# Kernel optimization log

Hardware: AMD Instinct MI355X
Metric: run time of the kernel (lower is better)

## Reference

```python
import jax, jax.numpy as jnp
import numpy as np

B, N, M, F_DIM, H, D = 4, 2048, 2048, 512, 8, 64  # M == num_time
MID = H * D
EPS = 1e-5


def _layernorm(x, w, b):
    mu = jnp.mean(x, axis=-1, keepdims=True)
    var = jnp.var(x, axis=-1, keepdims=True)
    return (x - mu) * jax.lax.rsqrt(var + EPS) * w + b


def setup_inputs() -> dict:
    key = jax.random.key(0)
    ks = jax.random.split(key, 12)
    s = 0.02
    return {
        "x": jax.random.normal(ks[0], (B, N, F_DIM), jnp.float32),
        "context": jax.random.normal(ks[1], (B, M, F_DIM), jnp.float32),
        "pos_emb": jax.random.normal(ks[2], (M, F_DIM), jnp.float32) * s,  # nn.Embedding(num_time, features)
        "ln_w": jnp.ones((F_DIM,), jnp.float32),
        "ln_b": jnp.zeros((F_DIM,), jnp.float32),
        "lnc_w": jnp.ones((F_DIM,), jnp.float32),
        "lnc_b": jnp.zeros((F_DIM,), jnp.float32),
        "Wq": jax.random.normal(ks[3], (F_DIM, MID), jnp.float32) * s,
        "Wk": jax.random.normal(ks[4], (F_DIM, MID), jnp.float32) * s,
        "Wv": jax.random.normal(ks[5], (F_DIM, MID), jnp.float32) * s,
        "Wout": jax.random.normal(ks[6], (MID, F_DIM), jnp.float32) * s,
        "bout": jnp.zeros((F_DIM,), jnp.float32),
    }


def reference(x, context, pos_emb, ln_w, ln_b, lnc_w, lnc_b, Wq, Wk, Wv, Wout, bout):
    scale = D ** (-0.5)
    keys = jnp.broadcast_to(pos_emb[None], (x.shape[0], M, F_DIM))  # [B, T, F]
    xn = _layernorm(x, ln_w, ln_b)
    kn = _layernorm(keys, ln_w, ln_b)          # same norm as x (self.norm)
    cn = _layernorm(context, lnc_w, lnc_b)
    q = (xn @ Wq).reshape(x.shape[0], N, H, D).transpose(0, 2, 1, 3)  # b h n d
    k = (kn @ Wk).reshape(x.shape[0], M, H, D).transpose(0, 2, 1, 3)  # b h m d
    v = (cn @ Wv).reshape(x.shape[0], M, H, D).transpose(0, 2, 1, 3)  # b h m d
    sim = jnp.einsum('bhnd,bhmd->bhnm', q, k) * scale
    attn = jax.nn.softmax(sim, axis=-1)
    out = jnp.einsum('bhnm,bhmd->bhnd', attn, v)
    out = out.transpose(0, 2, 1, 3).reshape(x.shape[0], N, MID)  # b n (h d)
    return out @ Wout + bout
```

## Files before the change

kernel.cpp:

```cpp
#include <hip/hip_runtime.h>
#include <stdint.h>

#define B_ 4
#define N_ 2048
#define M_ 2048
#define F_ 512
#define H_ 8
#define D_ 64

typedef __bf16 bf16x8 __attribute__((ext_vector_type(8)));
typedef float f32x4 __attribute__((ext_vector_type(4)));
typedef float f32x16 __attribute__((ext_vector_type(16)));

typedef const __attribute__((address_space(1))) uint32_t* gas_ptr;
typedef __attribute__((address_space(3))) uint32_t* las_ptr;

__device__ inline ushort f32_bf16(float f) {
    union { float f; uint32_t u; } v; v.f = f;
    uint32_t r = v.u + 0x7FFFu + ((v.u >> 16) & 1u);
    return (ushort)(r >> 16);
}

__global__ __launch_bounds__(128) void ln_kernel(
    const float* __restrict__ x, const float* __restrict__ ctx, const float* __restrict__ pos,
    const float* __restrict__ lnw, const float* __restrict__ lnb,
    const float* __restrict__ lncw, const float* __restrict__ lncb,
    ushort* __restrict__ xn, ushort* __restrict__ kn, ushort* __restrict__ cn)
{
    int r = blockIdx.x;
    const float* src; ushort* dst; const float* w; const float* bp;
    if (r < B_ * N_) {
        src = x + (size_t)r * F_; dst = xn + (size_t)r * F_; w = lnw; bp = lnb;
    } else if (r < B_ * N_ + M_) {
        int rr = r - B_ * N_;
        src = pos + (size_t)rr * F_; dst = kn + (size_t)rr * F_; w = lnw; bp = lnb;
    } else {
        int rr = r - (B_ * N_ + M_);
        src = ctx + (size_t)rr * F_; dst = cn + (size_t)rr * F_; w = lncw; bp = lncb;
    }
    int tid = threadIdx.x;
    int wave = tid >> 6, lane = tid & 63;
    float4 v = reinterpret_cast<const float4*>(src)[tid];
    float s = v.x + v.y + v.z + v.w;
    float sq = v.x * v.x + v.y * v.y + v.z * v.z + v.w * v.w;
    #pragma unroll
    for (int mask = 1; mask < 64; mask <<= 1) {
        s += __shfl_xor(s, mask, 64);
        sq += __shfl_xor(sq, mask, 64);
    }
    __shared__ float red[4];
    if (lane == 0) { red[wave * 2] = s; red[wave * 2 + 1] = sq; }
    __syncthreads();
    float S = red[0] + red[2], SQ = red[1] + red[3];
    float mean = S * (1.0f / F_);
    float var = SQ * (1.0f / F_) - mean * mean;
    float rstd = rsqrtf(var + 1e-5f);
    float4 wv = reinterpret_cast<const float4*>(w)[tid];
    float4 bv = reinterpret_cast<const float4*>(bp)[tid];
    ushort4 o;
    o.x = f32_bf16((v.x - mean) * rstd * wv.x + bv.x);
    o.y = f32_bf16((v.y - mean) * rstd * wv.y + bv.y);
    o.z = f32_bf16((v.z - mean) * rstd * wv.z + bv.z);
    o.w = f32_bf16((v.w - mean) * rstd * wv.w + bv.w);
    reinterpret_cast<ushort4*>(dst)[tid] = o;
}

__global__ __launch_bounds__(256) void wtrans_kernel(
    const float* __restrict__ Wq, const float* __restrict__ Wk,
    const float* __restrict__ Wv, const float* __restrict__ Wo,
    ushort* __restrict__ WqT, ushort* __restrict__ WkT,
    ushort* __restrict__ WvT, ushort* __restrict__ WoT)
{
    const float* W; ushort* WT;
    switch (blockIdx.z) {
        case 0: W = Wq; WT = WqT; break;
        case 1: W = Wk; WT = WkT; break;
        case 2: W = Wv; WT = WvT; break;
        default: W = Wo; WT = WoT; break;
    }
    __shared__ float tile[32][33];
    int tx = threadIdx.x, ty = threadIdx.y;
    int n0 = blockIdx.x * 32, k0 = blockIdx.y * 32;
    #pragma unroll
    for (int j = 0; j < 4; ++j)
        tile[ty + j * 8][tx] = W[(size_t)(k0 + ty + j * 8) * F_ + n0 + tx];
    __syncthreads();
    #pragma unroll
    for (int j = 0; j < 4; ++j)
        WT[(size_t)(n0 + ty + j * 8) * F_ + k0 + tx] = f32_bf16(tile[tx][ty + j * 8]);
}

__device__ __forceinline__ void gemm_body(
    const ushort* __restrict__ A, const ushort* __restrict__ BT,
    const float* __restrict__ bias, void* __restrict__ Cout,
    int mode, int bx, int by)
{
    __shared__ ushort As[128][64];
    __shared__ ushort Bs[128][64];
    int tid = threadIdx.x;
    int row0 = by * 128, col0 = bx * 128;
    int wv = tid >> 6, lane = tid & 63;
    int wm = wv >> 1, wn = wv & 1;
    f32x4 acc[4][4] = {};

    const int lrow8 = lane >> 3;
    const int chs = ((lane & 7) ^ (lrow8 & 7)) * 8;
    const ushort* agp = A + (size_t)(row0 + wv * 32 + lrow8) * F_ + chs;
    const ushort* bgp = BT + (size_t)(col0 + wv * 32 + lrow8) * F_ + chs;

    for (int k0 = 0; k0 < F_; k0 += 64) {
        #pragma unroll
        for (int j = 0; j < 4; ++j) {
            __builtin_amdgcn_global_load_lds(
                (gas_ptr)(const void*)(agp + k0 + j * 8 * F_),
                (las_ptr)(void*)&As[wv * 32 + j * 8][0], 16, 0, 0);
            __builtin_amdgcn_global_load_lds(
                (gas_ptr)(const void*)(bgp + k0 + j * 8 * F_),
                (las_ptr)(void*)&Bs[wv * 32 + j * 8][0], 16, 0, 0);
        }
        __syncthreads();
        #pragma unroll
        for (int kt = 0; kt < 2; ++kt) {
            int lrow = lane & 15;
            int ch = ((kt * 4 + (lane >> 4)) ^ (lane & 7)) * 8;
            bf16x8 af[4], bfr[4];
            #pragma unroll
            for (int mt = 0; mt < 4; ++mt)
                af[mt] = *reinterpret_cast<const bf16x8*>(&As[wm * 64 + mt * 16 + lrow][ch]);
            #pragma unroll
            for (int nt = 0; nt < 4; ++nt)
                bfr[nt] = *reinterpret_cast<const bf16x8*>(&Bs[wn * 64 + nt * 16 + lrow][ch]);
            #pragma unroll
            for (int mt = 0; mt < 4; ++mt)
                #pragma unroll
                for (int nt = 0; nt < 4; ++nt)
                    acc[mt][nt] = __builtin_amdgcn_mfma_f32_16x16x32_bf16(
                        af[mt], bfr[nt], acc[mt][nt], 0, 0, 0);
        }
        __syncthreads();
    }

    int lr4 = (lane >> 4) * 4, lc = lane & 15;
    #pragma unroll
    for (int mt = 0; mt < 4; ++mt) {
        #pragma unroll
        for (int nt = 0; nt < 4; ++nt) {
            int ccol = col0 + wn * 64 + nt * 16 + lc;
            float bv = (mode == 1) ? bias[ccol] : 0.0f;
            #pragma unroll
            for (int j = 0; j < 4; ++j) {
                int crow = row0 + wm * 64 + mt * 16 + lr4 + j;
                float val = acc[mt][nt][j] + bv;
                if (mode == 1) {
                    reinterpret_cast<float*>(Cout)[(size_t)crow * F_ + ccol] = val;
                } else if (mode == 0) {
                    reinterpret_cast<ushort*>(Cout)[(size_t)crow * F_ + ccol] = f32_bf16(val);
                } else if (mode == 2) {
                    int h = ccol >> 6, t = crow >> 7, s = (crow >> 6) & 1;
                    int ab = (crow >> 5) & 1, l31 = crow & 31;
                    int ds = (ccol >> 4) & 3, g2 = (ccol >> 3) & 1, e = ccol & 7;
                    size_t addr = (((size_t)(h * 16 + t) * 16 + s * 8 + ds * 2 + ab) * 64
                                   + g2 * 32 + l31) * 8 + e;
                    reinterpret_cast<ushort*>(Cout)[addr] = f32_bf16(val);
                } else {
                    int b2 = crow >> 11, m = crow & 2047;
                    int h = ccol >> 6, d = ccol & 63;
                    int bh = b2 * 8 + h, hh = d >> 5, l31 = d & 31;
                    int t = m >> 7, s = (m >> 6) & 1, s_ = (m >> 4) & 3;
                    int g2 = (m >> 3) & 1, i = m & 7;
                    size_t addr = (((size_t)(bh * 16 + t) * 16 + hh * 8 + s * 4 + s_) * 64
                                   + g2 * 32 + l31) * 8 + i;
                    reinterpret_cast<ushort*>(Cout)[addr] = f32_bf16(val);
                }
            }
        }
    }
}

__global__ __launch_bounds__(256) void qkv_gemm_kernel(
    const ushort* __restrict__ xn, const ushort* __restrict__ kn,
    const ushort* __restrict__ cn,
    const ushort* __restrict__ WqT, const ushort* __restrict__ WkT,
    const ushort* __restrict__ WvT,
    ushort* __restrict__ qb, ushort* __restrict__ kF, ushort* __restrict__ vF)
{
    int bid = blockIdx.x;
    if (bid < 256) {
        gemm_body(xn, WqT, nullptr, (void*)qb, 0, bid & 3, bid >> 2);
    } else if (bid < 320) {
        int t = bid - 256;
        gemm_body(kn, WkT, nullptr, (void*)kF, 2, t & 3, t >> 2);
    } else {
        int t = bid - 320;
        gemm_body(cn, WvT, nullptr, (void*)vF, 3, t & 3, t >> 2);
    }
}

__global__ __launch_bounds__(256) void out_gemm_kernel(
    const ushort* __restrict__ A, const ushort* __restrict__ WoT,
    const float* __restrict__ bias, float* __restrict__ out)
{
    gemm_body(A, WoT, bias, (void*)out, 1, blockIdx.x & 3, blockIdx.x >> 2);
}

#define MAKE_PA(dst, p, ss) do {                                               \
    uint32_t w0_, w1_, w2_, w3_;                                               \
    asm("v_cvt_pk_bf16_f32 %0, %1, %2" : "=v"(w0_) : "v"(p[8*(ss)+0]), "v"(p[8*(ss)+1])); \
    asm("v_cvt_pk_bf16_f32 %0, %1, %2" : "=v"(w1_) : "v"(p[8*(ss)+2]), "v"(p[8*(ss)+3])); \
    asm("v_cvt_pk_bf16_f32 %0, %1, %2" : "=v"(w2_) : "v"(p[8*(ss)+4]), "v"(p[8*(ss)+5])); \
    asm("v_cvt_pk_bf16_f32 %0, %1, %2" : "=v"(w3_) : "v"(p[8*(ss)+6]), "v"(p[8*(ss)+7])); \
    asm("v_permlane32_swap_b32 %0, %1" : "+v"(w0_), "+v"(w2_));                \
    asm("v_permlane32_swap_b32 %0, %1" : "+v"(w1_), "+v"(w3_));                \
    union { uint32_t w[4]; bf16x8 v; } u_;                                     \
    u_.w[0] = w0_; u_.w[1] = w1_; u_.w[2] = w2_; u_.w[3] = w3_;                \
    dst = u_.v;                                                                \
} while (0)

#define KLOAD(DST, u) do {                                                     \
    const ushort* _p = kfb_ + (size_t)(u) * 4096 + lane * 8;                   \
    _Pragma("unroll")                                                          \
    for (int f_ = 0; f_ < 8; ++f_)                                             \
        DST[f_] = *reinterpret_cast<const bf16x8*>(_p + f_ * 512);             \
} while (0)

#define VLOAD(DST, u) do {                                                     \
    const ushort* _p = vfb_ + (size_t)((u) >> 1) * 8192 +                      \
                       ((u) & 1) * 4 * 512 + lane * 8;                         \
    _Pragma("unroll")                                                          \
    for (int hh_ = 0; hh_ < 2; ++hh_)                                          \
        _Pragma("unroll")                                                      \
        for (int s2_ = 0; s2_ < 4; ++s2_)                                      \
            DST[hh_ * 4 + s2_] = *reinterpret_cast<const bf16x8*>(             \
                _p + (hh_ * 8 + s2_) * 512);                                   \
} while (0)

#define COMPUTE(KR, VR) do {                                                   \
    f32x16 sA, sB;                                                             \
    _Pragma("unroll")                                                          \
    for (int j = 0; j < 16; ++j) { sA[j] = 0.0f; sB[j] = 0.0f; }               \
    __builtin_amdgcn_s_setprio(1);                                             \
    _Pragma("unroll")                                                          \
    for (int ds_ = 0; ds_ < 4; ++ds_) {                                        \
        sA = __builtin_amdgcn_mfma_f32_32x32x16_bf16(KR[ds_ * 2], qf[ds_], sA, 0, 0, 0); \
        sB = __builtin_amdgcn_mfma_f32_32x32x16_bf16(KR[ds_ * 2 + 1], qf[ds_], sB, 0, 0, 0); \
    }                                                                          \
    __builtin_amdgcn_s_setprio(0);                                             \
    float p0f[16], p1f[16];                                                    \
    _Pragma("unroll")                                                          \
    for (int j = 0; j < 16; ++j)                                               \
        p0f[j] = __builtin_amdgcn_exp2f(sA[j] * c1);                           \
    _Pragma("unroll")                                                          \
    for (int j = 0; j < 16; ++j)                                               \
        p1f[j] = __builtin_amdgcn_exp2f(sB[j] * c1);                           \
    float r0 = 0.0f, r1 = 0.0f, r2 = 0.0f, r3 = 0.0f;                          \
    _Pragma("unroll")                                                          \
    for (int j = 0; j < 16; j += 4) {                                          \
        r0 += p0f[j];     r1 += p0f[j + 1];                                    \
        r2 += p0f[j + 2]; r3 += p0f[j + 3];                                    \
    }                                                                          \
    _Pragma("unroll")                                                          \
    for (int j = 0; j < 16; j += 4) {                                          \
        r0 += p1f[j];     r1 += p1f[j + 1];                                    \
        r2 += p1f[j + 2]; r3 += p1f[j + 3];                                    \
    }                                                                          \
    l_run += (r0 + r1) + (r2 + r3);                                            \
    bf16x8 pa[4];                                                               \
    MAKE_PA(pa[0], p0f, 0);                                                    \
    MAKE_PA(pa[1], p0f, 1);                                                    \
    MAKE_PA(pa[2], p1f, 0);                                                    \
    MAKE_PA(pa[3], p1f, 1);                                                    \
    __builtin_amdgcn_s_setprio(1);                                             \
    _Pragma("unroll")                                                          \
    for (int hh = 0; hh < 2; ++hh)                                             \
        _Pragma("unroll")                                                      \
        for (int s_ = 0; s_ < 4; ++s_)                                         \
            oacc[hh] = __builtin_amdgcn_mfma_f32_32x32x16_bf16(                \
                pa[s_], VR[hh * 4 + s_], oacc[hh], 0, 0, 0);                   \
    __builtin_amdgcn_s_setprio(0);                                             \
} while (0)

__global__ __launch_bounds__(512, 2) void attn_kernel(
    const ushort* __restrict__ q,
    const ushort* __restrict__ kF,
    const ushort* __restrict__ vF,
    ushort* __restrict__ o)
{
    const int wave = threadIdx.x >> 6, lane = threadIdx.x & 63;
    const int l31 = lane & 31, g = lane >> 5;
    const int qsub = wave & 1, quarter = wave >> 1;
    const int bh = blockIdx.y, b = bh >> 3, h = bh & 7;
    const int q0 = blockIdx.x * 64 + qsub * 32;

    __shared__ float ols[2][2][32][64];
    __shared__ float lls[2][2][64];

    bf16x8 qf[4];
    const ushort* qrow = q + (size_t)(b * N_ + q0 + l31) * F_ + h * 64 + g * 8;
    #pragma unroll
    for (int ds = 0; ds < 4; ++ds)
        qf[ds] = *reinterpret_cast<const bf16x8*>(qrow + ds * 16);

    float l_run = 0.0f;
    f32x16 oacc[2];
    #pragma unroll
    for (int hh = 0; hh < 2; ++hh)
        #pragma unroll
        for (int j = 0; j < 16; ++j) oacc[hh][j] = 0.0f;

    const ushort* kfb_ = kF + (size_t)h * 16 * 16 * 512;
    const ushort* vfb_ = vF + (size_t)bh * 16 * 16 * 512;
    const float c1 = 0.18033688f;

    bf16x8 kR[8], vR[8];
    const int ubase = quarter * 8;

    #pragma unroll 1
    for (int uu = 0; uu < 8; ++uu) {
        int u = ubase + uu;
        KLOAD(kR, u);
        VLOAD(vR, u);
        COMPUTE(kR, vR);
    }

    float lfull = l_run + __shfl_xor(l_run, 32, 64);

    if (quarter & 1) {
        int slot = quarter >> 1;
        #pragma unroll
        for (int hh = 0; hh < 2; ++hh)
            #pragma unroll
            for (int j = 0; j < 16; ++j)
                ols[qsub][slot][hh * 16 + j][lane] = oacc[hh][j];
        lls[qsub][slot][lane] = lfull;
    }
    __syncthreads();
    if (!(quarter & 1)) {
        int slot = quarter >> 1;
        #pragma unroll
        for (int hh = 0; hh < 2; ++hh)
            #pragma unroll
            for (int j = 0; j < 16; ++j)
                oacc[hh][j] += ols[qsub][slot][hh * 16 + j][lane];
        lfull += lls[qsub][slot][lane];
    }
    __syncthreads();
    if (quarter == 2) {
        #pragma unroll
        for (int hh = 0; hh < 2; ++hh)
            #pragma unroll
            for (int j = 0; j < 16; ++j)
                ols[qsub][0][hh * 16 + j][lane] = oacc[hh][j];
        lls[qsub][0][lane] = lfull;
    }
    __syncthreads();
    if (quarter == 0) {
        #pragma unroll
        for (int hh = 0; hh < 2; ++hh)
            #pragma unroll
            for (int j = 0; j < 16; ++j)
                oacc[hh][j] += ols[qsub][0][hh * 16 + j][lane];
        lfull += lls[qsub][0][lane];
        float linv = 1.0f / lfull;
        float rli[16];
        #pragma unroll
        for (int j = 0; j < 16; ++j)
            rli[j] = __shfl(linv, 8 * (j >> 2) + 4 * g + (j & 3), 64);
        #pragma unroll
        for (int hh = 0; hh < 2; ++hh)
            #pragma unroll
            for (int j = 0; j < 16; ++j) {
                int qr = (j & 3) + 8 * (j >> 2) + 4 * g;
                o[(size_t)(b * N_ + q0 + qr) * F_ + h * 64 + hh * 32 + l31] =
                    f32_bf16(oacc[hh][j] * rli[j]);
            }
    }
}

extern "C" void kernel_launch(void* const* d_in, const int* in_sizes, int n_in,
                              void* d_out, int out_size, void* d_ws, size_t ws_size,
                              hipStream_t stream) {
    const float* x    = (const float*)d_in[0];
    const float* ctx  = (const float*)d_in[1];
    const float* pos  = (const float*)d_in[2];
    const float* lnw  = (const float*)d_in[3];
    const float* lnb  = (const float*)d_in[4];
    const float* lncw = (const float*)d_in[5];
    const float* lncb = (const float*)d_in[6];
    const float* Wq   = (const float*)d_in[7];
    const float* Wk   = (const float*)d_in[8];
    const float* Wv   = (const float*)d_in[9];
    const float* Wo   = (const float*)d_in[10];
    const float* bout = (const float*)d_in[11];
    float* out = (float*)d_out;

    char* ws = (char*)d_ws;
    ushort* xn  = (ushort*)(ws + 0);
    ushort* cn  = (ushort*)(ws + 8388608);
    ushort* kn  = (ushort*)(ws + 16777216);
    ushort* WqT = (ushort*)(ws + 18874368);
    ushort* WkT = (ushort*)(ws + 19398656);
    ushort* WvT = (ushort*)(ws + 19922944);
    ushort* WoT = (ushort*)(ws + 20447232);
    ushort* qb  = (ushort*)(ws + 20971520);
    ushort* kFb = (ushort*)(ws + 29360128);
    ushort* vFb = (ushort*)(ws + 39845888);
    ushort* ao  = (ushort*)(ws + 48234496);

    hipLaunchKernelGGL(ln_kernel, dim3(B_ * N_ + M_ + B_ * M_), dim3(128), 0, stream,
                       x, ctx, pos, lnw, lnb, lncw, lncb, xn, kn, cn);
    hipLaunchKernelGGL(wtrans_kernel, dim3(16, 16, 4), dim3(32, 8), 0, stream,
                       Wq, Wk, Wv, Wo, WqT, WkT, WvT, WoT);
    hipLaunchKernelGGL(qkv_gemm_kernel, dim3(576), dim3(256), 0, stream,
                       xn, kn, cn, WqT, WkT, WvT, qb, kFb, vFb);
    hipLaunchKernelGGL(attn_kernel, dim3(32, 32), dim3(512), 0, stream,
                       qb, kFb, vFb, ao);
    hipLaunchKernelGGL(out_gemm_kernel, dim3(256), dim3(256), 0, stream,
                       ao, WoT, bout, out);
}
```

Baseline: 108.7 us.

## Process two 32-row query tiles per wave to reuse K/V fragments

Each wave now holds two 32-row query fragments and runs the QK/PV compute for both on every K/V fragment it loads. This halves K/V global loads per query row. Waves split the key range into two halves instead of four, and the cross-wave reduction drops from three barrier stages to one. Each block now covers 256 queries, so the grid shrinks from 32x32 to 8x32 blocks. The price is higher register pressure (two accumulators, the launch_bounds occupancy hint removed) and fewer blocks, which may cut occupancy and load balance across CUs.

Result: faster. 104.0 us (-4.3%).

```diff
diff --git a/kernel.cpp b/kernel.cpp
--- a/kernel.cpp
+++ b/kernel.cpp
@@ -234,15 +234,15 @@
                 _p + (hh_ * 8 + s2_) * 512);                                   \
 } while (0)
 
-#define COMPUTE(KR, VR) do {                                                   \
+#define COMPUTE_ONE(QF, OACC, LR) do {                                         \
     f32x16 sA, sB;                                                             \
     _Pragma("unroll")                                                          \
     for (int j = 0; j < 16; ++j) { sA[j] = 0.0f; sB[j] = 0.0f; }               \
     __builtin_amdgcn_s_setprio(1);                                             \
     _Pragma("unroll")                                                          \
     for (int ds_ = 0; ds_ < 4; ++ds_) {                                        \
-        sA = __builtin_amdgcn_mfma_f32_32x32x16_bf16(KR[ds_ * 2], qf[ds_], sA, 0, 0, 0); \
-        sB = __builtin_amdgcn_mfma_f32_32x32x16_bf16(KR[ds_ * 2 + 1], qf[ds_], sB, 0, 0, 0); \
+        sA = __builtin_amdgcn_mfma_f32_32x32x16_bf16(kR[ds_ * 2], QF[ds_], sA, 0, 0, 0); \
+        sB = __builtin_amdgcn_mfma_f32_32x32x16_bf16(kR[ds_ * 2 + 1], QF[ds_], sB, 0, 0, 0); \
     }                                                                          \
     __builtin_amdgcn_s_setprio(0);                                             \
     float p0f[16], p1f[16];                                                    \
@@ -263,8 +263,8 @@
         r0 += p1f[j];     r1 += p1f[j + 1];                                    \
         r2 += p1f[j + 2]; r3 += p1f[j + 3];                                    \
     }                                                                          \
-    l_run += (r0 + r1) + (r2 + r3);                                            \
-    bf16x8 pa[4];                                                               \
+    LR += (r0 + r1) + (r2 + r3);                                               \
+    bf16x8 pa[4];                                                              \
     MAKE_PA(pa[0], p0f, 0);                                                    \
     MAKE_PA(pa[1], p0f, 1);                                                    \
     MAKE_PA(pa[2], p1f, 0);                                                    \
@@ -274,12 +274,12 @@
     for (int hh = 0; hh < 2; ++hh)                                             \
         _Pragma("unroll")                                                      \
         for (int s_ = 0; s_ < 4; ++s_)                                         \
-            oacc[hh] = __builtin_amdgcn_mfma_f32_32x32x16_bf16(                \
-                pa[s_], VR[hh * 4 + s_], oacc[hh], 0, 0, 0);                   \
+            OACC[hh] = __builtin_amdgcn_mfma_f32_32x32x16_bf16(                \
+                pa[s_], vR[hh * 4 + s_], OACC[hh], 0, 0, 0);                   \
     __builtin_amdgcn_s_setprio(0);                                             \
 } while (0)
 
-__global__ __launch_bounds__(512, 2) void attn_kernel(
+__global__ __launch_bounds__(512) void attn_kernel(
     const ushort* __restrict__ q,
     const ushort* __restrict__ kF,
     const ushort* __restrict__ vF,
@@ -287,91 +287,87 @@
 {
     const int wave = threadIdx.x >> 6, lane = threadIdx.x & 63;
     const int l31 = lane & 31, g = lane >> 5;
-    const int qsub = wave & 1, quarter = wave >> 1;
+    const int qpair = wave & 3, half = wave >> 2;
     const int bh = blockIdx.y, b = bh >> 3, h = bh & 7;
-    const int q0 = blockIdx.x * 64 + qsub * 32;
-
-    __shared__ float ols[2][2][32][64];
-    __shared__ float lls[2][2][64];
-
-    bf16x8 qf[4];
-    const ushort* qrow = q + (size_t)(b * N_ + q0 + l31) * F_ + h * 64 + g * 8;
-    #pragma unroll
-    for (int ds = 0; ds < 4; ++ds)
-        qf[ds] = *reinterpret_cast<const bf16x8*>(qrow + ds * 16);
-
-    float l_run = 0.0f;
-    f32x16 oacc[2];
+    const int q0 = blockIdx.x * 256 + qpair * 64;
+
+    __shared__ float ols[4][64][64];
+    __shared__ float lls[4][2][64];
+
+    bf16x8 qfA[4], qfB[4];
+    const ushort* qrowA = q + (size_t)(b * N_ + q0 + l31) * F_ + h * 64 + g * 8;
+    const ushort* qrowB = qrowA + 32 * F_;
+    #pragma unroll
+    for (int ds = 0; ds < 4; ++ds) {
+        qfA[ds] = *reinterpret_cast<const bf16x8*>(qrowA + ds * 16);
+        qfB[ds] = *reinterpret_cast<const bf16x8*>(qrowB + ds * 16);
+    }
+
+    float l0 = 0.0f, l1 = 0.0f;
+    f32x16 oaccA[2], oaccB[2];
     #pragma unroll
     for (int hh = 0; hh < 2; ++hh)
         #pragma unroll
-        for (int j = 0; j < 16; ++j) oacc[hh][j] = 0.0f;
+        for (int j = 0; j < 16; ++j) { oaccA[hh][j] = 0.0f; oaccB[hh][j] = 0.0f; }
 
     const ushort* kfb_ = kF + (size_t)h * 16 * 16 * 512;
     const ushort* vfb_ = vF + (size_t)bh * 16 * 16 * 512;
     const float c1 = 0.18033688f;
 
     bf16x8 kR[8], vR[8];
-    const int ubase = quarter * 8;
+    const int ubase = half * 16;
 
     #pragma unroll 1
-    for (int uu = 0; uu < 8; ++uu) {
+    for (int uu = 0; uu < 16; ++uu) {
         int u = ubase + uu;
         KLOAD(kR, u);
         VLOAD(vR, u);
-        COMPUTE(kR, vR);
-    }
-
-    float lfull = l_run + __shfl_xor(l_run, 32, 64);
-
-    if (quarter & 1) {
-        int slot = quarter >> 1;
+        COMPUTE_ONE(qfA, oaccA, l0);
+        COMPUTE_ONE(qfB, oaccB, l1);
+    }
+
+    l0 += __shfl_xor(l0, 32, 64);
+    l1 += __shfl_xor(l1, 32, 64);
+
+    if (half) {
         #pragma unroll
         for (int hh = 0; hh < 2; ++hh)
             #pragma unroll
-            for (int j = 0; j < 16; ++j)
-                ols[qsub][slot][hh * 16 + j][lane] = oacc[hh][j];
-        lls[qsub][slot][lane] = lfull;
+            for (int j = 0; j < 16; ++j) {
+                ols[qpair][hh * 16 + j][lane] = oaccA[hh][j];
+                ols[qpair][32 + hh * 16 + j][lane] = oaccB[hh][j];
+            }
+        lls[qpair][0][lane] = l0;
+        lls[qpair][1][lane] = l1;
     }
     __syncthreads();
-    if (!(quarter & 1)) {
-        int slot = quarter >> 1;
+    if (!half) {
         #pragma unroll
         for (int hh = 0; hh < 2; ++hh)
             #pragma unroll
-            for (int j = 0; j < 16; ++j)
-                oacc[hh][j] += ols[qsub][slot][hh * 16 + j][lane];
-        lfull += lls[qsub][slot][lane];
-    }
-    __syncthreads();
-    if (quarter == 2) {
-        #pragma unroll
-        for (int hh = 0; hh < 2; ++hh)
-            #pragma unroll
-            for (int j = 0; j < 16; ++j)
-                ols[qsub][0][hh * 16 + j][lane] = oacc[hh][j];
-        lls[qsub][0][lane] = lfull;
-    }
-    __syncthreads();
-    if (quarter == 0) {
-        #pragma unroll
-        for (int hh = 0; hh < 2; ++hh)
-            #pragma unroll
-            for (int j = 0; j < 16; ++j)
-                oacc[hh][j] += ols[qsub][0][hh * 16 + j][lane];
-        lfull += lls[qsub][0][lane];
-        float linv = 1.0f / lfull;
-        float rli[16];
-        #pragma unroll
-        for (int j = 0; j < 16; ++j)
-            rli[j] = __shfl(linv, 8 * (j >> 2) + 4 * g + (j & 3), 64);
+            for (int j = 0; j < 16; ++j) {
+                oaccA[hh][j] += ols[qpair][hh * 16 + j][lane];
+                oaccB[hh][j] += ols[qpair][32 + hh * 16 + j][lane];
+            }
+        l0 += lls[qpair][0][lane];
+        l1 += lls[qpair][1][lane];
+        float li0 = 1.0f / l0, li1 = 1.0f / l1;
+        float rli0[16], rli1[16];
+        #pragma unroll
+        for (int j = 0; j < 16; ++j) {
+            int idx = 8 * (j >> 2) + 4 * g + (j & 3);
+            rli0[j] = __shfl(li0, idx, 64);
+            rli1[j] = __shfl(li1, idx, 64);
+        }
         #pragma unroll
         for (int hh = 0; hh < 2; ++hh)
             #pragma unroll
             for (int j = 0; j < 16; ++j) {
                 int qr = (j & 3) + 8 * (j >> 2) + 4 * g;
                 o[(size_t)(b * N_ + q0 + qr) * F_ + h * 64 + hh * 32 + l31] =
-                    f32_bf16(oacc[hh][j] * rli[j]);
+                    f32_bf16(oaccA[hh][j] * rli0[j]);
+                o[(size_t)(b * N_ + q0 + 32 + qr) * F_ + h * 64 + hh * 32 + l31] =
+                    f32_bf16(oaccB[hh][j] * rli1[j]);
             }
     }
 }
@@ -412,7 +408,7 @@
                        Wq, Wk, Wv, Wo, WqT, WkT, WvT, WoT);
     hipLaunchKernelGGL(qkv_gemm_kernel, dim3(576), dim3(256), 0, stream,
                        xn, kn, cn, WqT, WkT, WvT, qb, kFb, vFb);
-    hipLaunchKernelGGL(attn_kernel, dim3(32, 32), dim3(512), 0, stream,
+    hipLaunchKernelGGL(attn_kernel, dim3(8, 32), dim3(512), 0, stream,
                        qb, kFb, vFb, ao);
     hipLaunchKernelGGL(out_gemm_kernel, dim3(256), dim3(256), 0, stream,
                        ao, WoT, bout, out);
```
